# Optimization experiments

Measured on AMD Instinct MI355X. Metric: run time of the kernel, lower is better.

## Reference

```python
import jax, jax.numpy as jnp
import numpy as np

N = 50000      # nodes
E = 500000     # edges (before self-loops)
D = 384        # in_channels == hidden3*6 (residual constraint)
H1, C1 = 4, 96   # conv1: heads, out_channels  -> 384
H2, C2 = 4, 96   # conv2 -> 384
H3, C3 = 6, 64   # conv3 -> 384
B = 64           # graphs in batch
SLOPE = 0.2      # GATConv leaky_relu negative_slope (PyG default)
LN_EPS = 1e-5


def _gat_params(key, fin, heads, c, scale=0.05):
    k1, k2, k3 = jax.random.split(key, 3)
    return dict(
        W=jax.random.normal(k1, (fin, heads * c), jnp.float32) * scale,
        a_src=jax.random.normal(k2, (heads, c), jnp.float32) * scale,
        a_dst=jax.random.normal(k3, (heads, c), jnp.float32) * scale,
        b=jnp.zeros((heads * c,), jnp.float32),
    )


def setup_inputs() -> dict:
    key = jax.random.key(0)
    ks = jax.random.split(key, 8)
    x = jax.random.normal(ks[0], (N, D), jnp.float32)
    edge_index = jax.random.randint(ks[1], (2, E), 0, N).astype(jnp.int64)
    batch = jnp.sort(jax.random.randint(ks[2], (N,), 0, B)).astype(jnp.int64)
    p1 = _gat_params(ks[3], D, H1, C1)
    p2 = _gat_params(ks[4], H1 * C1, H2, C2)
    p3 = _gat_params(ks[5], H2 * C2, H3, C3)
    return {
        'x': x, 'edge_index': edge_index, 'batch': batch,
        'W1': p1['W'], 'a1_src': p1['a_src'], 'a1_dst': p1['a_dst'], 'b1': p1['b'],
        'g1': jnp.ones((H1 * C1,), jnp.float32), 'be1': jnp.zeros((H1 * C1,), jnp.float32),
        'W2': p2['W'], 'a2_src': p2['a_src'], 'a2_dst': p2['a_dst'], 'b2': p2['b'],
        'g2': jnp.ones((H2 * C2,), jnp.float32), 'be2': jnp.zeros((H2 * C2,), jnp.float32),
        'W3': p3['W'], 'a3_src': p3['a_src'], 'a3_dst': p3['a_dst'], 'b3': p3['b'],
    }


def _layer_norm(x, g, b):
    mu = jnp.mean(x, axis=-1, keepdims=True)
    var = jnp.mean(jnp.square(x - mu), axis=-1, keepdims=True)
    return (x - mu) * jax.lax.rsqrt(var + LN_EPS) * g + b


def _gat_conv(x, src, dst, W, a_src, a_dst, b, heads, c):
    # h: [N, H, C] projected features (shared W across heads, PyG-style)
    h = (x @ W).reshape(N, heads, c)
    s_src = jnp.einsum('nhc,hc->nh', h, a_src)   # [N, H]
    s_dst = jnp.einsum('nhc,hc->nh', h, a_dst)
    e = jax.nn.leaky_relu(s_src[src] + s_dst[dst], SLOPE)  # [E', H]
    # segment softmax over incoming edges of each dst (self-loops guarantee coverage)
    e_max = jax.ops.segment_max(e, dst, num_segments=N)
    e = jnp.exp(e - e_max[dst])
    denom = jax.ops.segment_sum(e, dst, num_segments=N)
    alpha = e / (denom[dst] + 1e-16)                        # [E', H]
    out = jax.ops.segment_sum(h[src] * alpha[:, :, None], dst, num_segments=N)
    return out.reshape(N, heads * c) + b


def reference(x, edge_index, batch,
              W1, a1_src, a1_dst, b1, g1, be1,
              W2, a2_src, a2_dst, b2, g2, be2,
              W3, a3_src, a3_dst, b3):
    # PyG GATConv adds self-loops by default
    ar = jnp.arange(N, dtype=edge_index.dtype)
    ei = jnp.concatenate([edge_index, jnp.stack([ar, ar])], axis=1)
    src, dst = ei[0], ei[1]

    x1 = _gat_conv(x, src, dst, W1, a1_src, a1_dst, b1, H1, C1)
    x1 = jax.nn.relu(_layer_norm(x1, g1, be1))
    x2 = _gat_conv(x1, src, dst, W2, a2_src, a2_dst, b2, H2, C2)
    x2 = jax.nn.relu(_layer_norm(x2, g2, be2))
    x3 = _gat_conv(x2, src, dst, W3, a3_src, a3_dst, b3, H3, C3)
    x3 = jax.nn.relu(x3)

    x_res = x + x3
    # global_mean_pool over batch assignment (dropout is identity at eval)
    sums = jax.ops.segment_sum(x_res, batch, num_segments=B)
    counts = jax.ops.segment_sum(jnp.ones((N,), x.dtype), batch, num_segments=B)
    return sums / jnp.maximum(counts, 1.0)[:, None]
```

## Files before the change

### kernel.cpp

```cpp
#include <hip/hip_runtime.h>

#define NNODES 50000
#define NEDGES 500000
#define DIM    384
#define NB     64
#define SLOPE  0.2f
#define LN_EPS 1e-5f
#define EPRIME (NEDGES + NNODES)
#define POOLS  16
#define SCANB  256
#define NSCB   ((NNODES + SCANB - 1) / SCANB)

typedef __attribute__((ext_vector_type(8))) short short8;
typedef __attribute__((ext_vector_type(4))) float floatx4;
typedef __attribute__((ext_vector_type(2))) float floatx2;

__device__ __forceinline__ int load_i(const void* p, long long i, int is64) {
  return is64 ? (int)((const long long*)p)[i] : ((const int*)p)[i];
}
__device__ __forceinline__ unsigned short f2bf(float f) {
  unsigned u = __float_as_uint(f);
  u += 0x7fffu + ((u >> 16) & 1u);
  return (unsigned short)(u >> 16);
}
__device__ __forceinline__ float bf2f(unsigned short u) {
  return __uint_as_float(((unsigned)u) << 16);
}

__global__ void detect_kernel(const int* __restrict__ ei32, int* __restrict__ flag) {
  __shared__ int nz;
  if (threadIdx.x == 0) nz = 0;
  __syncthreads();
  if (ei32[2 * threadIdx.x + 1] != 0) atomicAdd(&nz, 1);
  __syncthreads();
  if (threadIdx.x == 0) *flag = (nz == 0) ? 1 : 0;
}

__global__ void count_kernel(const void* __restrict__ ei, const int* __restrict__ flag,
                             int* __restrict__ deg) {
  int is64 = *flag;
  for (int i = blockIdx.x * blockDim.x + threadIdx.x; i < EPRIME; i += gridDim.x * blockDim.x) {
    int d = (i < NEDGES) ? load_i(ei, (long long)NEDGES + i, is64) : (i - NEDGES);
    atomicAdd(&deg[d], 1);
  }
}

__global__ void scan1_kernel(const int* __restrict__ deg, int* __restrict__ row_ptr,
                             int* __restrict__ btot) {
  __shared__ int buf[SCANB];
  int t = threadIdx.x, idx = blockIdx.x * SCANB + t;
  int v = (idx < NNODES) ? deg[idx] : 0;
  buf[t] = v;
  __syncthreads();
  for (int off = 1; off < SCANB; off <<= 1) {
    int x = (t >= off) ? buf[t - off] : 0;
    __syncthreads();
    buf[t] += x;
    __syncthreads();
  }
  if (idx < NNODES) row_ptr[idx] = buf[t] - v;
  if (t == SCANB - 1) btot[blockIdx.x] = buf[t];
}
__global__ void scan2_kernel(int* __restrict__ btot) {
  __shared__ int buf[256];
  int t = threadIdx.x;
  int v = (t < NSCB) ? btot[t] : 0;
  buf[t] = v;
  __syncthreads();
  for (int off = 1; off < 256; off <<= 1) {
    int x = (t >= off) ? buf[t - off] : 0;
    __syncthreads();
    buf[t] += x;
    __syncthreads();
  }
  if (t < NSCB) btot[t] = buf[t] - v;
}
__global__ void scan3_kernel(int* __restrict__ row_ptr, int* __restrict__ cursor,
                             const int* __restrict__ btot) {
  int idx = blockIdx.x * SCANB + threadIdx.x;
  if (idx < NNODES) {
    int v = row_ptr[idx] + btot[blockIdx.x];
    row_ptr[idx] = v;
    cursor[idx] = v;
  }
  if (idx == 0) row_ptr[NNODES] = EPRIME;
}

__global__ void scatter_kernel(const void* __restrict__ ei, const int* __restrict__ flag,
                               int* __restrict__ cursor, int* __restrict__ srt) {
  int is64 = *flag;
  for (int i = blockIdx.x * blockDim.x + threadIdx.x; i < EPRIME; i += gridDim.x * blockDim.x) {
    int s, d;
    if (i < NEDGES) { s = load_i(ei, i, is64); d = load_i(ei, (long long)NEDGES + i, is64); }
    else            { s = d = i - NEDGES; }
    int pos = atomicAdd(&cursor[d], 1);
    srt[pos] = s;
  }
}

__global__ void convert_x_kernel(const float* __restrict__ x, unsigned short* __restrict__ xb) {
  int i = blockIdx.x * blockDim.x + threadIdx.x;
  float4 v = ((const float4*)x)[i];
  ushort4 o;
  o.x = f2bf(v.x); o.y = f2bf(v.y); o.z = f2bf(v.z); o.w = f2bf(v.w);
  ((ushort4*)xb)[i] = o;
}

__global__ void convert_w_kernel(const float* __restrict__ W1, const float* __restrict__ W2,
                                 const float* __restrict__ W3, unsigned short* __restrict__ Wt) {
  const float* W = (blockIdx.y == 0) ? W1 : (blockIdx.y == 1) ? W2 : W3;
  unsigned short* o = Wt + (size_t)blockIdx.y * DIM * DIM;
  int n = blockIdx.x;
  int k = threadIdx.x;
  o[n * DIM + k] = f2bf(W[k * DIM + n]);
}

__global__ __launch_bounds__(256)
void gemm_bf16_kernel(const unsigned short* __restrict__ A,
                      const unsigned short* __restrict__ Bt,
                      unsigned char* __restrict__ C8, int M) {
  __shared__ unsigned short As[128 * 32];
  __shared__ unsigned short Bs[128 * 32];
  int tid = threadIdx.x;
  int lane = tid & 63;
  int wave = tid >> 6;
  int bm = blockIdx.x * 128;
  int bn = blockIdx.y * 128;
  int wm = (wave & 1) * 64;
  int wn = (wave >> 1) * 64;
  int l16 = lane & 15;
  int lq  = lane >> 4;

  floatx4 acc[4][4];
#pragma unroll
  for (int mi = 0; mi < 4; ++mi)
#pragma unroll
    for (int ni = 0; ni < 4; ++ni)
      acc[mi][ni] = (floatx4){0.f, 0.f, 0.f, 0.f};

  for (int k0 = 0; k0 < DIM; k0 += 32) {
    __syncthreads();
#pragma unroll
    for (int i = 0; i < 2; ++i) {
      int c = i * 256 + tid;
      int r = c >> 2;
      int col = (c & 3) << 3;
      int ra = bm + r; if (ra >= M) ra = M - 1;
      __builtin_amdgcn_global_load_lds(
          (const __attribute__((address_space(1))) void*)(A + (size_t)ra * DIM + k0 + col),
          (__attribute__((address_space(3))) void*)(As + c * 8), 16, 0, 0);
      __builtin_amdgcn_global_load_lds(
          (const __attribute__((address_space(1))) void*)(Bt + (size_t)(bn + r) * DIM + k0 + col),
          (__attribute__((address_space(3))) void*)(Bs + c * 8), 16, 0, 0);
    }
    __syncthreads();
    short8 av[4], bv[4];
#pragma unroll
    for (int mi = 0; mi < 4; ++mi)
      av[mi] = *(const short8*)&As[(wm + mi * 16 + l16) * 32 + lq * 8];
#pragma unroll
    for (int ni = 0; ni < 4; ++ni)
      bv[ni] = *(const short8*)&Bs[(wn + ni * 16 + l16) * 32 + lq * 8];
#pragma unroll
    for (int mi = 0; mi < 4; ++mi)
#pragma unroll
      for (int ni = 0; ni < 4; ++ni)
        acc[mi][ni] = __builtin_amdgcn_mfma_f32_16x16x32_bf16(av[mi], bv[ni], acc[mi][ni], 0, 0, 0);
  }

#pragma unroll
  for (int mi = 0; mi < 4; ++mi) {
#pragma unroll
    for (int r = 0; r < 4; ++r) {
      int row = bm + wm + mi * 16 + lq * 4 + r;
      if (row < M) {
#pragma unroll
        for (int ni = 0; ni < 4; ++ni) {
          float fv = acc[mi][ni][r];
          int pk = __builtin_amdgcn_cvt_pk_fp8_f32(fv, fv, 0, false);
          C8[(size_t)row * DIM + bn + wn + ni * 16 + l16] = (unsigned char)(pk & 0xff);
        }
      }
    }
  }
}

template <int H>
__global__ __launch_bounds__(256)
void score_kernel(const unsigned char* __restrict__ h8,
                  const float* __restrict__ asrc, const float* __restrict__ adst,
                  float* __restrict__ ssrc, float* __restrict__ sdst) {
  constexpr int LPH = 48 / H;
  int wave = threadIdx.x >> 6, lane = threadIdx.x & 63;
  int n = blockIdx.x * 4 + wave;
  bool colane = lane < 48;
  int lc = min(lane, 47);
  int j = lc * 8;

  __shared__ float r1[4][64], r2[4][64];
  float s1 = 0.f, s2 = 0.f;
  if (colane) {
    uint2 pk = *(const uint2*)(h8 + (size_t)n * DIM + j);
    floatx2 p0 = __builtin_amdgcn_cvt_pk_f32_fp8((int)pk.x, false);
    floatx2 p1 = __builtin_amdgcn_cvt_pk_f32_fp8((int)pk.x, true);
    floatx2 p2 = __builtin_amdgcn_cvt_pk_f32_fp8((int)pk.y, false);
    floatx2 p3 = __builtin_amdgcn_cvt_pk_f32_fp8((int)pk.y, true);
    float f[8] = {p0.x, p0.y, p1.x, p1.y, p2.x, p2.y, p3.x, p3.y};
    float4 a0 = *(const float4*)(asrc + j);
    float4 a1 = *(const float4*)(asrc + j + 4);
    float4 d0 = *(const float4*)(adst + j);
    float4 d1 = *(const float4*)(adst + j + 4);
    s1 = f[0]*a0.x + f[1]*a0.y + f[2]*a0.z + f[3]*a0.w
       + f[4]*a1.x + f[5]*a1.y + f[6]*a1.z + f[7]*a1.w;
    s2 = f[0]*d0.x + f[1]*d0.y + f[2]*d0.z + f[3]*d0.w
       + f[4]*d1.x + f[5]*d1.y + f[6]*d1.z + f[7]*d1.w;
  }
  r1[wave][lane] = colane ? s1 : 0.f;
  r2[wave][lane] = colane ? s2 : 0.f;
  asm volatile("s_waitcnt lgkmcnt(0)" ::: "memory");
  __builtin_amdgcn_wave_barrier();
  if (lane < H) {
    float a = 0.f;
#pragma unroll
    for (int k = 0; k < LPH; ++k) a += r1[wave][lane * LPH + k];
    ssrc[n * H + lane] = a;
  } else if (lane >= 8 && lane < 8 + H) {
    int h = lane - 8;
    float a = 0.f;
#pragma unroll
    for (int k = 0; k < LPH; ++k) a += r2[wave][h * LPH + k];
    sdst[n * H + h] = a;
  }
}

template <int H, int MODE>
__global__ __launch_bounds__(256)
void aggregate_kernel(const int* __restrict__ row_ptr, const int* __restrict__ srt,
                      const float* __restrict__ ssrc, const float* __restrict__ sdst,
                      const unsigned char* __restrict__ h8, const float* __restrict__ bias,
                      const float* __restrict__ gamma, const float* __restrict__ beta,
                      const unsigned short* __restrict__ xresb,
                      unsigned short* __restrict__ outb) {
  constexpr int C = DIM / H;
  int wave = threadIdx.x >> 6;
  int lane = threadIdx.x & 63;
  int n = blockIdx.x * 4 + wave;
  int start = row_ptr[n];
  int deg = row_ptr[n + 1] - start;

  bool colane = lane < 48;
  int lc = min(lane, 47);
  int j = lc * 8;
  int myhead = j / C;

  int ww_i8 = min(lane / H, 7);
  int ww_i4 = min(lane / H, 3);
  int ww_h  = lane % H;

  float sd  = sdst[n * H + myhead];
  float sdw = sdst[n * H + ww_h];

  float acc[8];
#pragma unroll
  for (int i = 0; i < 8; ++i) acc[i] = 0.f;
  float den = 0.f;

  const int* sp = srt + start;

  auto accum = [&](uint2 pk, float w) {
    floatx2 p0 = __builtin_amdgcn_cvt_pk_f32_fp8((int)pk.x, false);
    floatx2 p1 = __builtin_amdgcn_cvt_pk_f32_fp8((int)pk.x, true);
    floatx2 p2 = __builtin_amdgcn_cvt_pk_f32_fp8((int)pk.y, false);
    floatx2 p3 = __builtin_amdgcn_cvt_pk_f32_fp8((int)pk.y, true);
    acc[0] = fmaf(w, p0.x, acc[0]); acc[1] = fmaf(w, p0.y, acc[1]);
    acc[2] = fmaf(w, p1.x, acc[2]); acc[3] = fmaf(w, p1.y, acc[3]);
    acc[4] = fmaf(w, p2.x, acc[4]); acc[5] = fmaf(w, p2.y, acc[5]);
    acc[6] = fmaf(w, p3.x, acc[6]); acc[7] = fmaf(w, p3.y, acc[7]);
  };
  auto wexp = [&](float f) {
    float v = f + sdw;
    v = fmaxf(v, SLOPE * v);
    return __expf(v);
  };

  int ee = 0;
  for (; ee + 8 <= deg; ee += 8) {
    int msrc = sp[ee + ww_i8];
    float sv = ssrc[msrc * H + ww_h];
    int s[8];
#pragma unroll
    for (int i = 0; i < 8; ++i) s[i] = __builtin_amdgcn_readfirstlane(sp[ee + i]);
    uint2 k[8];
#pragma unroll
    for (int i = 0; i < 8; ++i) k[i] = *(const uint2*)(h8 + (size_t)s[i] * DIM + j);
    float wv = wexp(sv);
#pragma unroll
    for (int i = 0; i < 8; ++i) {
      float w = __shfl(wv, i * H + myhead);
      den += w;
      accum(k[i], w);
    }
  }
  for (; ee + 4 <= deg; ee += 4) {
    int msrc = sp[ee + ww_i4];
    float sv = ssrc[msrc * H + ww_h];
    int s[4];
#pragma unroll
    for (int i = 0; i < 4; ++i) s[i] = __builtin_amdgcn_readfirstlane(sp[ee + i]);
    uint2 k[4];
#pragma unroll
    for (int i = 0; i < 4; ++i) k[i] = *(const uint2*)(h8 + (size_t)s[i] * DIM + j);
    float wv = wexp(sv);
#pragma unroll
    for (int i = 0; i < 4; ++i) {
      float w = __shfl(wv, i * H + myhead);
      den += w;
      accum(k[i], w);
    }
  }
  for (; ee < deg; ++ee) {
    int su = __builtin_amdgcn_readfirstlane(sp[ee]);
    uint2 pk = *(const uint2*)(h8 + (size_t)su * DIM + j);
    float v = ssrc[su * H + myhead] + sd;
    v = fmaxf(v, SLOPE * v);
    float w = __expf(v);
    den += w;
    accum(pk, w);
  }

  float invden = 1.f / (den + 1e-16f);
  float v[8];
  float4 b0 = *(const float4*)(bias + j);
  float4 b1 = *(const float4*)(bias + j + 4);
  v[0] = acc[0] * invden + b0.x; v[1] = acc[1] * invden + b0.y;
  v[2] = acc[2] * invden + b0.z; v[3] = acc[3] * invden + b0.w;
  v[4] = acc[4] * invden + b1.x; v[5] = acc[5] * invden + b1.y;
  v[6] = acc[6] * invden + b1.z; v[7] = acc[7] * invden + b1.w;

  if (MODE == 0) {
    float s1 = 0.f, s2 = 0.f;
    if (colane) {
#pragma unroll
      for (int i = 0; i < 8; ++i) { s1 += v[i]; s2 += v[i] * v[i]; }
    }
#pragma unroll
    for (int off = 32; off > 0; off >>= 1) {
      s1 += __shfl_xor(s1, off);
      s2 += __shfl_xor(s2, off);
    }
    float mu = s1 * (1.f / DIM);
    float var = s2 * (1.f / DIM) - mu * mu;
    float rs = rsqrtf(var + LN_EPS);
    if (colane) {
      float4 g0 = *(const float4*)(gamma + j);
      float4 g1 = *(const float4*)(gamma + j + 4);
      float4 e0 = *(const float4*)(beta + j);
      float4 e1 = *(const float4*)(beta + j + 4);
      float gg[8] = {g0.x, g0.y, g0.z, g0.w, g1.x, g1.y, g1.z, g1.w};
      float bb[8] = {e0.x, e0.y, e0.z, e0.w, e1.x, e1.y, e1.z, e1.w};
      ushort4 o0, o1;
      unsigned short oy[8];
#pragma unroll
      for (int i = 0; i < 8; ++i) {
        float y = (v[i] - mu) * rs * gg[i] + bb[i];
        oy[i] = f2bf(fmaxf(y, 0.f));
      }
      o0.x = oy[0]; o0.y = oy[1]; o0.z = oy[2]; o0.w = oy[3];
      o1.x = oy[4]; o1.y = oy[5]; o1.z = oy[6]; o1.w = oy[7];
      *(ushort4*)(outb + (size_t)n * DIM + j) = o0;
      *(ushort4*)(outb + (size_t)n * DIM + j + 4) = o1;
    }
  } else {
    if (colane) {
      uint4 xp = *(const uint4*)(xresb + (size_t)n * DIM + j);
      float xf[8];
      xf[0] = __uint_as_float(xp.x << 16); xf[1] = __uint_as_float(xp.x & 0xffff0000u);
      xf[2] = __uint_as_float(xp.y << 16); xf[3] = __uint_as_float(xp.y & 0xffff0000u);
      xf[4] = __uint_as_float(xp.z << 16); xf[5] = __uint_as_float(xp.z & 0xffff0000u);
      xf[6] = __uint_as_float(xp.w << 16); xf[7] = __uint_as_float(xp.w & 0xffff0000u);
      ushort4 o0, o1;
      unsigned short oy[8];
#pragma unroll
      for (int i = 0; i < 8; ++i) oy[i] = f2bf(fmaxf(v[i], 0.f) + xf[i]);
      o0.x = oy[0]; o0.y = oy[1]; o0.z = oy[2]; o0.w = oy[3];
      o1.x = oy[4]; o1.y = oy[5]; o1.z = oy[6]; o1.w = oy[7];
      *(ushort4*)(outb + (size_t)n * DIM + j) = o0;
      *(ushort4*)(outb + (size_t)n * DIM + j + 4) = o1;
    }
  }
}

__global__ void pool_kernel(const unsigned short* __restrict__ xr, const void* __restrict__ batch,
                            const int* __restrict__ flag, float* __restrict__ out) {
  int b = blockIdx.x;
  int s = blockIdx.y;
  int t = threadIdx.x;
  int is64 = *flag;
  int lo, hi;
  { int l = 0, r = NNODES;
    while (l < r) { int m = (l + r) >> 1; if (load_i(batch, m, is64) < b) l = m + 1; else r = m; }
    lo = l; }
  { int l = lo, r = NNODES;
    while (l < r) { int m = (l + r) >> 1; if (load_i(batch, m, is64) < b + 1) l = m + 1; else r = m; }
    hi = l; }
  int cnt = hi - lo;
  float inv = 1.f / (float)max(cnt, 1);
  int chunk = (cnt + POOLS - 1) / POOLS;
  int r0 = lo + s * chunk;
  int r1 = min(r0 + chunk, hi);
  float acc = 0.f;
  for (int nn = r0; nn < r1; ++nn) acc += bf2f(xr[(size_t)nn * DIM + t]);
  if (r1 > r0) atomicAdd(&out[b * DIM + t], acc * inv);
}

extern "C" void kernel_launch(void* const* d_in, const int* in_sizes, int n_in,
                              void* d_out, int out_size, void* d_ws, size_t ws_size,
                              hipStream_t stream) {
  const float* x    = (const float*)d_in[0];
  const void*  ei   = d_in[1];
  const void*  batch= d_in[2];
  const float* W1   = (const float*)d_in[3];
  const float* a1s  = (const float*)d_in[4];
  const float* a1d  = (const float*)d_in[5];
  const float* b1   = (const float*)d_in[6];
  const float* g1   = (const float*)d_in[7];
  const float* be1  = (const float*)d_in[8];
  const float* W2   = (const float*)d_in[9];
  const float* a2s  = (const float*)d_in[10];
  const float* a2d  = (const float*)d_in[11];
  const float* b2   = (const float*)d_in[12];
  const float* g2   = (const float*)d_in[13];
  const float* be2  = (const float*)d_in[14];
  const float* W3   = (const float*)d_in[15];
  const float* a3s  = (const float*)d_in[16];
  const float* a3d  = (const float*)d_in[17];
  const float* b3   = (const float*)d_in[18];
  float* out = (float*)d_out;

  char* ws = (char*)d_ws;
  size_t off = 0;
  auto alloc = [&](size_t bytes) -> void* {
    void* p = ws + off;
    off = (off + bytes + 255) & ~(size_t)255;
    return p;
  };
  int*   flag    = (int*)alloc(4);
  unsigned short* Xb = (unsigned short*)alloc((size_t)NNODES * DIM * 2);
  unsigned short* Qb = (unsigned short*)alloc((size_t)NNODES * DIM * 2);
  unsigned char*  P8 = (unsigned char*)alloc((size_t)NNODES * DIM);
  unsigned short* Wt = (unsigned short*)alloc((size_t)3 * DIM * DIM * 2);
  float* ssrc    = (float*)alloc((size_t)NNODES * 6 * 4);
  float* sdst    = (float*)alloc((size_t)NNODES * 6 * 4);
  int*   row_ptr = (int*)alloc((size_t)(NNODES + 1) * 4);
  int*   cursor  = (int*)alloc((size_t)NNODES * 4);
  int*   deg     = (int*)alloc((size_t)NNODES * 4);
  int*   btot    = (int*)alloc((size_t)NSCB * 4);
  int*   srt     = (int*)alloc((size_t)EPRIME * 4);

  detect_kernel<<<1, 256, 0, stream>>>((const int*)ei, flag);
  hipMemsetAsync(deg, 0, (size_t)NNODES * 4, stream);
  hipMemsetAsync(d_out, 0, (size_t)out_size * 4, stream);
  int eblocks = (EPRIME + 255) / 256;
  count_kernel<<<eblocks, 256, 0, stream>>>(ei, flag, deg);
  scan1_kernel<<<NSCB, SCANB, 0, stream>>>(deg, row_ptr, btot);
  scan2_kernel<<<1, 256, 0, stream>>>(btot);
  scan3_kernel<<<NSCB, SCANB, 0, stream>>>(row_ptr, cursor, btot);
  scatter_kernel<<<eblocks, 256, 0, stream>>>(ei, flag, cursor, srt);

  convert_x_kernel<<<(NNODES * DIM / 4 + 255) / 256, 256, 0, stream>>>(x, Xb);
  convert_w_kernel<<<dim3(DIM, 3), DIM, 0, stream>>>(W1, W2, W3, Wt);

  dim3 ggrid((NNODES + 127) / 128, DIM / 128);
  int agrid = NNODES / 4;

  gemm_bf16_kernel<<<ggrid, 256, 0, stream>>>(Xb, Wt, P8, NNODES);
  score_kernel<4><<<agrid, 256, 0, stream>>>(P8, a1s, a1d, ssrc, sdst);
  aggregate_kernel<4, 0><<<agrid, 256, 0, stream>>>(row_ptr, srt, ssrc, sdst, P8, b1, g1, be1,
                                                    nullptr, Qb);
  gemm_bf16_kernel<<<ggrid, 256, 0, stream>>>(Qb, Wt + (size_t)DIM * DIM, P8, NNODES);
  score_kernel<4><<<agrid, 256, 0, stream>>>(P8, a2s, a2d, ssrc, sdst);
  aggregate_kernel<4, 0><<<agrid, 256, 0, stream>>>(row_ptr, srt, ssrc, sdst, P8, b2, g2, be2,
                                                    nullptr, Qb);
  gemm_bf16_kernel<<<ggrid, 256, 0, stream>>>(Qb, Wt + (size_t)2 * DIM * DIM, P8, NNODES);
  score_kernel<6><<<agrid, 256, 0, stream>>>(P8, a3s, a3d, ssrc, sdst);
  aggregate_kernel<6, 1><<<agrid, 256, 0, stream>>>(row_ptr, srt, ssrc, sdst, P8, b3, nullptr,
                                                    nullptr, Xb, Qb);
  pool_kernel<<<dim3(NB, POOLS), DIM, 0, stream>>>(Qb, batch, flag, out);
}
```

Before: 522.8 us.

## Preload neighbor indices into lanes and double-buffer gathers in GAT aggregation

Each wave now loads up to 64 neighbor indices into registers once and reads them with readlane/shfl, instead of issuing repeated scalar loads from the CSR array. The 8-edge main loop is software-pipelined with two register buffers, so the next batch of fp8 feature gathers is in flight while the current one is accumulated. Aggregation blocks shrink from 4 waves to 2 to give finer scheduling granularity. The extra buffer raises register pressure and may lower occupancy. Nodes with more than 64 neighbours fall back to the old serial loop.

Result: slower. 551.2 us (+5.4%).

```diff
diff --git a/kernel.cpp b/kernel.cpp
--- a/kernel.cpp
+++ b/kernel.cpp
@@ -234,7 +234,7 @@
 }
 
 template <int H, int MODE>
-__global__ __launch_bounds__(256)
+__global__ __launch_bounds__(128)
 void aggregate_kernel(const int* __restrict__ row_ptr, const int* __restrict__ srt,
                       const float* __restrict__ ssrc, const float* __restrict__ sdst,
                       const unsigned char* __restrict__ h8, const float* __restrict__ bias,
@@ -244,7 +244,7 @@
   constexpr int C = DIM / H;
   int wave = threadIdx.x >> 6;
   int lane = threadIdx.x & 63;
-  int n = blockIdx.x * 4 + wave;
+  int n = blockIdx.x * 2 + wave;
   int start = row_ptr[n];
   int deg = row_ptr[n + 1] - start;
 
@@ -266,6 +266,9 @@
   float den = 0.f;
 
   const int* sp = srt + start;
+
+  int myidx = sp[min(lane, deg - 1)];
+  int fast = min(deg, 64);
 
   auto accum = [&](uint2 pk, float w) {
     floatx2 p0 = __builtin_amdgcn_cvt_pk_f32_fp8((int)pk.x, false);
@@ -283,33 +286,56 @@
     return __expf(v);
   };
 
-  int ee = 0;
-  for (; ee + 8 <= deg; ee += 8) {
-    int msrc = sp[ee + ww_i8];
-    float sv = ssrc[msrc * H + ww_h];
-    int s[8];
-#pragma unroll
-    for (int i = 0; i < 8; ++i) s[i] = __builtin_amdgcn_readfirstlane(sp[ee + i]);
-    uint2 k[8];
-#pragma unroll
-    for (int i = 0; i < 8; ++i) k[i] = *(const uint2*)(h8 + (size_t)s[i] * DIM + j);
+  auto issue = [&](int ee, uint2 (&kk)[8], float& sv) {
+    int msrc = __shfl(myidx, ee + ww_i8);
+    sv = ssrc[msrc * H + ww_h];
+#pragma unroll
+    for (int i = 0; i < 8; ++i) {
+      int si = __builtin_amdgcn_readlane(myidx, ee + i);
+      kk[i] = *(const uint2*)(h8 + (size_t)si * DIM + j);
+    }
+  };
+  auto consume = [&](uint2 (&kk)[8], float sv) {
     float wv = wexp(sv);
 #pragma unroll
     for (int i = 0; i < 8; ++i) {
       float w = __shfl(wv, i * H + myhead);
       den += w;
-      accum(k[i], w);
-    }
-  }
-  for (; ee + 4 <= deg; ee += 4) {
-    int msrc = sp[ee + ww_i4];
+      accum(kk[i], w);
+    }
+  };
+
+  int ee = 0;
+  int nb8 = fast >> 3;
+  if (nb8 > 0) {
+    uint2 kA[8], kB[8];
+    float svA, svB;
+    issue(0, kA, svA);
+    int t = 1;
+    for (; t + 1 < nb8; t += 2) {
+      issue(t * 8, kB, svB);
+      consume(kA, svA);
+      issue((t + 1) * 8, kA, svA);
+      consume(kB, svB);
+    }
+    if (t < nb8) {
+      issue(t * 8, kB, svB);
+      consume(kA, svA);
+      consume(kB, svB);
+    } else {
+      consume(kA, svA);
+    }
+    ee = nb8 * 8;
+  }
+  if (ee + 4 <= fast) {
+    int msrc = __shfl(myidx, ee + ww_i4);
     float sv = ssrc[msrc * H + ww_h];
-    int s[4];
-#pragma unroll
-    for (int i = 0; i < 4; ++i) s[i] = __builtin_amdgcn_readfirstlane(sp[ee + i]);
     uint2 k[4];
 #pragma unroll
-    for (int i = 0; i < 4; ++i) k[i] = *(const uint2*)(h8 + (size_t)s[i] * DIM + j);
+    for (int i = 0; i < 4; ++i) {
+      int si = __builtin_amdgcn_readlane(myidx, ee + i);
+      k[i] = *(const uint2*)(h8 + (size_t)si * DIM + j);
+    }
     float wv = wexp(sv);
 #pragma unroll
     for (int i = 0; i < 4; ++i) {
@@ -317,6 +343,16 @@
       den += w;
       accum(k[i], w);
     }
+    ee += 4;
+  }
+  for (; ee < fast; ++ee) {
+    int si = __builtin_amdgcn_readlane(myidx, ee);
+    uint2 pk = *(const uint2*)(h8 + (size_t)si * DIM + j);
+    float v = ssrc[si * H + myhead] + sd;
+    v = fmaxf(v, SLOPE * v);
+    float w = __expf(v);
+    den += w;
+    accum(pk, w);
   }
   for (; ee < deg; ++ee) {
     int su = __builtin_amdgcn_readfirstlane(sp[ee]);
@@ -471,19 +507,19 @@
   convert_w_kernel<<<dim3(DIM, 3), DIM, 0, stream>>>(W1, W2, W3, Wt);
 
   dim3 ggrid((NNODES + 127) / 128, DIM / 128);
-  int agrid = NNODES / 4;
+  int agrid = NNODES / 2;
 
   gemm_bf16_kernel<<<ggrid, 256, 0, stream>>>(Xb, Wt, P8, NNODES);
-  score_kernel<4><<<agrid, 256, 0, stream>>>(P8, a1s, a1d, ssrc, sdst);
-  aggregate_kernel<4, 0><<<agrid, 256, 0, stream>>>(row_ptr, srt, ssrc, sdst, P8, b1, g1, be1,
+  score_kernel<4><<<NNODES / 4, 256, 0, stream>>>(P8, a1s, a1d, ssrc, sdst);
+  aggregate_kernel<4, 0><<<agrid, 128, 0, stream>>>(row_ptr, srt, ssrc, sdst, P8, b1, g1, be1,
                                                     nullptr, Qb);
   gemm_bf16_kernel<<<ggrid, 256, 0, stream>>>(Qb, Wt + (size_t)DIM * DIM, P8, NNODES);
-  score_kernel<4><<<agrid, 256, 0, stream>>>(P8, a2s, a2d, ssrc, sdst);
-  aggregate_kernel<4, 0><<<agrid, 256, 0, stream>>>(row_ptr, srt, ssrc, sdst, P8, b2, g2, be2,
+  score_kernel<4><<<NNODES / 4, 256, 0, stream>>>(P8, a2s, a2d, ssrc, sdst);
+  aggregate_kernel<4, 0><<<agrid, 128, 0, stream>>>(row_ptr, srt, ssrc, sdst, P8, b2, g2, be2,
                                                     nullptr, Qb);
   gemm_bf16_kernel<<<ggrid, 256, 0, stream>>>(Qb, Wt + (size_t)2 * DIM * DIM, P8, NNODES);
-  score_kernel<6><<<agrid, 256, 0, stream>>>(P8, a3s, a3d, ssrc, sdst);
-  aggregate_kernel<6, 1><<<agrid, 256, 0, stream>>>(row_ptr, srt, ssrc, sdst, P8, b3, nullptr,
+  score_kernel<6><<<NNODES / 4, 256, 0, stream>>>(P8, a3s, a3d, ssrc, sdst);
+  aggregate_kernel<6, 1><<<agrid, 128, 0, stream>>>(row_ptr, srt, ssrc, sdst, P8, b3, nullptr,
                                                     nullptr, Xb, Qb);
   pool_kernel<<<dim3(NB, POOLS), DIM, 0, stream>>>(Qb, batch, flag, out);
 }
```
